# Optimization experiments

Measured on AMD Instinct MI355X. Metric: run time of the kernel, lower is better.

The kernel has to match this reference:

```python
import jax, jax.numpy as jnp
import numpy as np

RADIUS = 0.1
NSAMPLE = 32
EPS = 1e-5


def ball_query(radius, nsample, xyz):
    # xyz: [B, N, 3] -> idx [B, N, nsample] (query set == support set)
    B, N, _ = xyz.shape
    # pairwise squared distances [B, N, N]
    sq = jnp.sum((xyz[:, :, None, :] - xyz[:, None, :, :]) ** 2, axis=-1)
    grp = jnp.broadcast_to(jnp.arange(N, dtype=jnp.int32), (B, N, N))
    grp = jnp.where(sq > radius * radius, N, grp)
    grp = jnp.sort(grp, axis=-1)[:, :, :nsample]
    first = grp[:, :, 0:1]
    return jnp.where(grp == N, first, grp)  # self is always in-ball -> first valid


def index_points(points, idx):
    # points [B, N, C], idx [B, N, S] -> [B, N, S, C]
    B, N, S = idx.shape
    C = points.shape[-1]
    flat = jnp.take_along_axis(points, idx.reshape(B, N * S, 1), axis=1)
    return flat.reshape(B, N, S, C)


def bn(x, gamma, beta, mean, var, axis):
    # eval-mode batchnorm over channel axis
    shape = [1] * x.ndim
    shape[axis] = -1
    g = gamma.reshape(shape); b = beta.reshape(shape)
    m = mean.reshape(shape); v = var.reshape(shape)
    return (x - m) * (g * jax.lax.rsqrt(v + EPS)) + b


def setup_inputs() -> dict:
    key = jax.random.key(0)
    ks = jax.random.split(key, 8)
    B, N, C, E = 4, 4096, 128, 4
    H = C * E
    xyz = jax.random.uniform(ks[0], (B, N, 3), dtype=jnp.float32)
    feats = jax.random.normal(ks[1], (B, N, C), dtype=jnp.float32)
    s = 0.05
    Wn = jax.random.normal(ks[2], (C, C + 3), dtype=jnp.float32) * s
    W1 = jax.random.normal(ks[3], (H, C), dtype=jnp.float32) * s
    W2 = jax.random.normal(ks[4], (C, H), dtype=jnp.float32) * s
    def bnp(k, n):
        k1, k2 = jax.random.split(k)
        return (jnp.ones((n,), jnp.float32) + 0.01 * jax.random.normal(k1, (n,)),
                0.01 * jax.random.normal(k2, (n,)),
                jnp.zeros((n,), jnp.float32),
                jnp.ones((n,), jnp.float32))
    gn, bn_, mn, vn = bnp(ks[5], C)
    g1, b1, m1, v1 = bnp(ks[6], H)
    g2, b2, m2, v2 = bnp(ks[7], C)
    return dict(xyz=xyz, feats=feats, Wn=Wn, gn=gn, bn_=bn_, mn=mn, vn=vn,
                W1=W1, g1=g1, b1=b1, m1=m1, v1=v1,
                W2=W2, g2=g2, b2=b2, m2=m2, v2=v2)


def reference(xyz, feats, Wn, gn, bn_, mn, vn, W1, g1, b1, m1, v1, W2, g2, b2, m2, v2):
    B, N, C = feats.shape
    identity = feats  # [B, N, C]
    idx = ball_query(RADIUS, NSAMPLE, xyz)  # [B, N, S]
    grouped_xyz = index_points(xyz, idx) - xyz[:, :, None, :]  # [B, N, S, 3]
    grouped_xyz = grouped_xyz / RADIUS  # normalize_dp
    grouped_feats = index_points(feats, idx)  # [B, N, S, C]
    grouped = jnp.concatenate([grouped_xyz, grouped_feats], axis=-1)  # [B, N, S, C+3]
    # torch layout [B, C+3, S, N]; keep [B, N, S, C+3] and contract channels
    x = jnp.einsum('oc,bnsc->bnso', Wn, grouped)  # neighbor 1x1 conv
    x = jax.nn.relu(bn(x, gn, bn_, mn, vn, axis=3))
    x = jnp.max(x, axis=2)  # max over neighbors -> [B, N, C]
    # inverted bottleneck pointwise MLP
    h = jnp.einsum('hc,bnc->bnh', W1, x)
    h = jax.nn.relu(bn(h, g1, b1, m1, v1, axis=2))
    y = jnp.einsum('ch,bnh->bnc', W2, h)
    y = bn(y, g2, b2, m2, v2, axis=2)
    out = jax.nn.relu(y + identity)  # [B, N, C]
    return out
```

## Files before the change

### kernel.cpp

```cpp
#include <hip/hip_runtime.h>
#include <hip/hip_bf16.h>
#include <math.h>

static constexpr int BB = 4;
static constexpr int NN = 4096;
static constexpr int CC = 128;
static constexpr int HH = 512;
static constexpr int SS = 32;
static constexpr float EPSF = 1e-5f;
static constexpr int NCELL = 1000;

typedef __bf16 bf16_t;
typedef bf16_t bf16x8 __attribute__((ext_vector_type(8)));
typedef float f32x4 __attribute__((ext_vector_type(4)));
typedef float f32x2 __attribute__((ext_vector_type(2)));

__device__ inline unsigned short f2bf(float f) {
    unsigned int u = __builtin_bit_cast(unsigned int, f);
    u += 0x7FFFu + ((u >> 16) & 1u);
    return (unsigned short)(u >> 16);
}
__device__ inline float u2f(unsigned int u) {
    return __builtin_bit_cast(float, u);
}
__device__ inline int cell_of(float v) {
    int c = (int)(v * 10.0f);
    return c > 9 ? 9 : (c < 0 ? 0 : c);
}
__device__ inline f32x2 pk_fma_b(f32x2 a, float g, f32x2 c) {
    const f32x2 gg = {g, g};
    return a * gg + c;
}

__device__ inline void gload_lds16(const void* g, void* l) {
    __builtin_amdgcn_global_load_lds(
        (const __attribute__((address_space(1))) unsigned int*)g,
        (__attribute__((address_space(3))) unsigned int*)l, 16, 0, 0);
}

__global__ __launch_bounds__(1024)
void prep_bin_kernel(const float* __restrict__ Wn, const float* __restrict__ W1,
                     const float* __restrict__ W2,
                     const float* __restrict__ gn, const float* __restrict__ bnv,
                     const float* __restrict__ mn, const float* __restrict__ vn,
                     const float* __restrict__ xyz,
                     unsigned short* __restrict__ WnF, unsigned short* __restrict__ W1b,
                     unsigned short* __restrict__ W2b, float4* __restrict__ wfold,
                     int* __restrict__ starts, float4* __restrict__ spts)
{
    const int blk = blockIdx.x;
    const int t   = threadIdx.x;

    __shared__ int cur[1024];
    __shared__ int ls[1024];

    if (blk < 144) {
        const int i = blk * 1024 + t;
        if (i < 16384) {
            const int o = i >> 7, c = i & 127;
            WnF[i] = f2bf(Wn[o * 131 + 3 + c]);
        } else if (i < 81920) {
            W1b[i - 16384] = f2bf(W1[i - 16384]);
        } else {
            W2b[i - 81920] = f2bf(W2[i - 81920]);
        }
        return;
    }
    if (blk == 144) {
        if (t < CC) {
            const float sc = gn[t] / sqrtf(vn[t] + EPSF);
            wfold[t] = make_float4(sc * Wn[t * 131 + 0], sc * Wn[t * 131 + 1],
                                   sc * Wn[t * 131 + 2], bnv[t] - mn[t] * sc);
        }
        return;
    }

    const int b = blk - 145;
    cur[t] = 0;
    __syncthreads();

    int    cid[4];
    float4 pt[4];
    #pragma unroll
    for (int k = 0; k < 4; ++k) {
        const int n = k * 1024 + t;
        const float x = xyz[((size_t)b * NN + n) * 3 + 0];
        const float y = xyz[((size_t)b * NN + n) * 3 + 1];
        const float z = xyz[((size_t)b * NN + n) * 3 + 2];
        cid[k] = cell_of(z) * 100 + cell_of(y) * 10 + cell_of(x);
        pt[k]  = make_float4(x, y, z, __int_as_float(n));
        atomicAdd(&cur[cid[k]], 1);
    }
    __syncthreads();

    const int v = cur[t];
    ls[t] = v;
    __syncthreads();
    #pragma unroll
    for (int off = 1; off < 1024; off <<= 1) {
        const int add = (t >= off) ? ls[t - off] : 0;
        __syncthreads();
        ls[t] += add;
        __syncthreads();
    }
    const int ex = ls[t] - v;
    if (t < NCELL) starts[b * NCELL + t] = b * NN + ex;
    if (b == 0 && t == 0) starts[BB * NCELL] = BB * NN;
    __syncthreads();
    cur[t] = ex;
    __syncthreads();

    #pragma unroll
    for (int k = 0; k < 4; ++k) {
        const int pos = atomicAdd(&cur[cid[k]], 1);
        spts[(size_t)b * NN + pos] = pt[k];
    }
}

__global__ __launch_bounds__(256, 2)
void tgemm_bq_kernel(const float* __restrict__ feats, const unsigned short* __restrict__ WnF,
                     const float* __restrict__ gn, const float* __restrict__ vn,
                     unsigned short* __restrict__ Tb,
                     const float* __restrict__ xyz, const int* __restrict__ starts,
                     const float4* __restrict__ spts, int* __restrict__ idx)
{
    __shared__ char smem[(64 + 128) * 128];

    if (blockIdx.x < 256) {
        char* sA = smem;
        char* sB = smem + 64 * 128;
        const int t    = threadIdx.x;
        const int lane = t & 63;
        const int w    = t >> 6;
        const int wm   = w >> 1;
        const int wn   = w & 1;
        const int m0   = blockIdx.x * 64;

        f32x4 acc[2][4];
        #pragma unroll
        for (int i = 0; i < 2; ++i)
            #pragma unroll
            for (int j = 0; j < 4; ++j) acc[i][j] = f32x4{0.f, 0.f, 0.f, 0.f};

        const char* Wb = (const char*)WnF;

        for (int kc = 0; kc < CC; kc += 64) {
            #pragma unroll
            for (int l = 0; l < 2; ++l) {
                const int q     = w * 2 + l;
                const int Lb    = q * 1024 + lane * 16;
                const int row   = Lb >> 7;
                const int inrow = Lb & 127;
                const int sw    = inrow ^ ((row & 7) << 4);
                const float* src = feats + (size_t)(m0 + row) * CC + kc + (sw >> 1);
                const float4 a0 = *(const float4*)(src);
                const float4 a1 = *(const float4*)(src + 4);
                uint4 pk;
                pk.x = (unsigned)f2bf(a0.x) | ((unsigned)f2bf(a0.y) << 16);
                pk.y = (unsigned)f2bf(a0.z) | ((unsigned)f2bf(a0.w) << 16);
                pk.z = (unsigned)f2bf(a1.x) | ((unsigned)f2bf(a1.y) << 16);
                pk.w = (unsigned)f2bf(a1.z) | ((unsigned)f2bf(a1.w) << 16);
                *(uint4*)(sA + Lb) = pk;
            }
            #pragma unroll
            for (int l = 0; l < 4; ++l) {
                const int q     = w * 4 + l;
                const int Lb    = q * 1024 + lane * 16;
                const int row   = Lb >> 7;
                const int inrow = Lb & 127;
                const char* src = Wb + (size_t)row * 256 + kc * 2 + (inrow ^ ((row & 7) << 4));
                gload_lds16(src, sB + q * 1024);
            }
            __syncthreads();

            #pragma unroll
            for (int ks = 0; ks < 2; ++ks) {
                const int kbyte = ks * 64 + (lane >> 4) * 16;
                bf16x8 af[2], bf[4];
                #pragma unroll
                for (int i = 0; i < 2; ++i) {
                    const int r = wm * 32 + i * 16 + (lane & 15);
                    af[i] = *(const bf16x8*)(sA + r * 128 + (kbyte ^ ((r & 7) << 4)));
                }
                #pragma unroll
                for (int j = 0; j < 4; ++j) {
                    const int r = wn * 64 + j * 16 + (lane & 15);
                    bf[j] = *(const bf16x8*)(sB + r * 128 + (kbyte ^ ((r & 7) << 4)));
                }
                #pragma unroll
                for (int i = 0; i < 2; ++i)
                    #pragma unroll
                    for (int j = 0; j < 4; ++j)
                        acc[i][j] = __builtin_amdgcn_mfma_f32_16x16x32_bf16(af[i], bf[j], acc[i][j], 0, 0, 0);
            }
            __syncthreads();
        }

        #pragma unroll
        for (int j = 0; j < 4; ++j) {
            const int col = wn * 64 + j * 16 + (lane & 15);
            const float scg = gn[col] / sqrtf(vn[col] + EPSF);
            #pragma unroll
            for (int i = 0; i < 2; ++i) {
                const int rowb = m0 + wm * 32 + i * 16 + (lane >> 4) * 4;
                #pragma unroll
                for (int r = 0; r < 4; ++r)
                    Tb[(size_t)(rowb + r) * CC + col] = f2bf(acc[i][j][r] * scg);
            }
        }
    } else {
        const int t    = threadIdx.x;
        const int wv   = t >> 6;
        const int lane = t & 63;
        const int p    = (blockIdx.x - 256) * 4 + wv;
        const int b    = p >> 12;

        int* lbase = (int*)smem + wv * 160;
        int* list  = lbase;
        int* res   = lbase + 128;

        const float qx = xyz[p * 3 + 0];
        const float qy = xyz[p * 3 + 1];
        const float qz = xyz[p * 3 + 2];
        const int cx = cell_of(qx), cy = cell_of(qy), cz = cell_of(qz);
        const int xlo = cx > 0 ? cx - 1 : 0;
        const int xhi = cx < 9 ? cx + 1 : 9;

        int cnt = 0;
        for (int dz = -1; dz <= 1; ++dz) {
            const int z2 = cz + dz;
            if (z2 < 0 || z2 > 9) continue;
            for (int dy = -1; dy <= 1; ++dy) {
                const int y2 = cy + dy;
                if (y2 < 0 || y2 > 9) continue;
                const int base = b * NCELL + z2 * 100 + y2 * 10;
                const int lo = starts[base + xlo];
                const int hi = starts[base + xhi + 1];
                for (int j0 = lo; j0 < hi; j0 += 64) {
                    const int j = j0 + lane;
                    bool in = false;
                    int pi = 0;
                    if (j < hi) {
                        const float4 s = spts[j];
                        float sq;
                        {
                            #pragma clang fp contract(off)
                            const float dx  = qx - s.x;
                            const float dyv = qy - s.y;
                            const float dzv = qz - s.z;
                            sq = dx * dx + dyv * dyv + dzv * dzv;
                        }
                        in = (sq <= 0.01f);
                        pi = __float_as_int(s.w);
                    }
                    const unsigned long long mask = __ballot(in);
                    if (in) {
                        const int pos = cnt + __popcll(mask & ((1ull << lane) - 1ull));
                        if (pos < 128) list[pos] = pi;
                    }
                    cnt += (int)__popcll(mask);
                }
            }
        }
        __syncthreads();

        const int c = cnt < 128 ? cnt : 128;
        #pragma unroll
        for (int l0 = 0; l0 < 2; ++l0) {
            const int l = lane + l0 * 64;
            if (l < c) {
                const int v = list[l];
                int r = 0;
                for (int k = 0; k < c; ++k) r += (list[k] < v);
                if (r < SS) res[r] = v;
            }
        }
        __syncthreads();

        if (lane < SS) {
            const int m = c < SS ? c : SS;
            idx[(size_t)p * SS + lane] = (lane < m) ? res[lane] : res[0];
        }
    }
}

__global__ __launch_bounds__(256)
void group_max_kernel(const float* __restrict__ xyz,
                      const unsigned short* __restrict__ T,
                      const float4* __restrict__ wfold,
                      const int* __restrict__ idx, unsigned short* __restrict__ xout)
{
    const int t   = threadIdx.x;
    const int ptl = t >> 5;
    const int l   = t & 31;
    const int p   = blockIdx.x * 8 + ptl;
    const int b   = p >> 12;

    __shared__ float4 sg[8][32];

    {
        const int j = idx[(size_t)p * SS + l];
        const float* q  = xyz + (size_t)p * 3;
        const float* pj = xyz + ((size_t)b * NN + j) * 3;
        sg[ptl][l] = make_float4((pj[0] - q[0]) / 0.1f,
                                 (pj[1] - q[1]) / 0.1f,
                                 (pj[2] - q[2]) / 0.1f, __int_as_float(j));
    }
    __syncthreads();

    const int c0 = l * 4;
    const float4 wa = wfold[c0 + 0], wb = wfold[c0 + 1];
    const float4 wc = wfold[c0 + 2], wd = wfold[c0 + 3];
    const f32x2 w0p0 = {wa.x, wb.x}, w1p0 = {wa.y, wb.y}, w2p0 = {wa.z, wb.z};
    const f32x2 w0p1 = {wc.x, wd.x}, w1p1 = {wc.y, wd.y}, w2p1 = {wc.z, wd.z};

    const unsigned short* Tbp = T + (size_t)b * NN * CC;
    f32x2 mx0 = {-1e30f, -1e30f}, mx1 = {-1e30f, -1e30f};

    #pragma unroll 8
    for (int s = 0; s < SS; ++s) {
        const float4 g = sg[ptl][s];
        const int j = __float_as_int(g.w);
        const uint2 tv = *(const uint2*)(Tbp + (size_t)j * CC + c0);
        f32x2 v0, v1;
        v0.x = u2f(tv.x << 16); v0.y = u2f(tv.x & 0xFFFF0000u);
        v1.x = u2f(tv.y << 16); v1.y = u2f(tv.y & 0xFFFF0000u);
        v0 = pk_fma_b(w0p0, g.x, v0); v0 = pk_fma_b(w1p0, g.y, v0); v0 = pk_fma_b(w2p0, g.z, v0);
        v1 = pk_fma_b(w0p1, g.x, v1); v1 = pk_fma_b(w1p1, g.y, v1); v1 = pk_fma_b(w2p1, g.z, v1);
        mx0.x = fmaxf(mx0.x, v0.x); mx0.y = fmaxf(mx0.y, v0.y);
        mx1.x = fmaxf(mx1.x, v1.x); mx1.y = fmaxf(mx1.y, v1.y);
    }

    const float r0 = fmaxf(mx0.x + wa.w, 0.f);
    const float r1 = fmaxf(mx0.y + wb.w, 0.f);
    const float r2 = fmaxf(mx1.x + wc.w, 0.f);
    const float r3 = fmaxf(mx1.y + wd.w, 0.f);
    uint2 o;
    o.x = (unsigned)f2bf(r0) | ((unsigned)f2bf(r1) << 16);
    o.y = (unsigned)f2bf(r2) | ((unsigned)f2bf(r3) << 16);
    *(uint2*)(xout + (size_t)p * CC + c0) = o;
}

template<int MODE, int BNt>
__global__ __launch_bounds__(256, 2)
void mfma_gemm_kernel(const unsigned short* __restrict__ A, const unsigned short* __restrict__ W,
                      const float* __restrict__ g, const float* __restrict__ bb,
                      const float* __restrict__ mu, const float* __restrict__ var,
                      const float* __restrict__ res, void* __restrict__ outv,
                      int M, int Nout, int K)
{
    constexpr int BM = 64, BK = 64;
    constexpr int NF = BNt / 32;
    __shared__ char smem[(BM + BNt) * BK * 2];
    char* sA = smem;
    char* sB = smem + BM * BK * 2;

    const int t    = threadIdx.x;
    const int lane = t & 63;
    const int w    = t >> 6;
    const int wm   = w >> 1;
    const int wn   = w & 1;
    const int m0   = blockIdx.x * BM;
    const int o0   = blockIdx.y * BNt;
    const int Kb   = K * 2;

    f32x4 acc[2][NF];
    #pragma unroll
    for (int i = 0; i < 2; ++i)
        #pragma unroll
        for (int j = 0; j < NF; ++j) acc[i][j] = f32x4{0.f, 0.f, 0.f, 0.f};

    const char* Ab = (const char*)A;
    const char* Wb = (const char*)W;

    for (int kc = 0; kc < K; kc += BK) {
        const int kcb = kc * 2;
        #pragma unroll
        for (int l = 0; l < 2; ++l) {
            const int q     = w * 2 + l;
            const int Lb    = q * 1024 + lane * 16;
            const int row   = Lb >> 7;
            const int inrow = Lb & 127;
            const char* src = Ab + (size_t)(m0 + row) * Kb + kcb + (inrow ^ ((row & 7) << 4));
            gload_lds16(src, sA + q * 1024);
        }
        #pragma unroll
        for (int l = 0; l < NF; ++l) {
            const int q     = w * NF + l;
            const int Lb    = q * 1024 + lane * 16;
            const int row   = Lb >> 7;
            const int inrow = Lb & 127;
            const char* src = Wb + (size_t)(o0 + row) * Kb + kcb + (inrow ^ ((row & 7) << 4));
            gload_lds16(src, sB + q * 1024);
        }
        __syncthreads();

        #pragma unroll
        for (int ks = 0; ks < 2; ++ks) {
            const int kbyte = ks * 64 + (lane >> 4) * 16;
            bf16x8 af[2], bf[NF];
            #pragma unroll
            for (int i = 0; i < 2; ++i) {
                const int r = wm * 32 + i * 16 + (lane & 15);
                af[i] = *(const bf16x8*)(sA + r * 128 + (kbyte ^ ((r & 7) << 4)));
            }
            #pragma unroll
            for (int j = 0; j < NF; ++j) {
                const int r = wn * (BNt / 2) + j * 16 + (lane & 15);
                bf[j] = *(const bf16x8*)(sB + r * 128 + (kbyte ^ ((r & 7) << 4)));
            }
            #pragma unroll
            for (int i = 0; i < 2; ++i)
                #pragma unroll
                for (int j = 0; j < NF; ++j)
                    acc[i][j] = __builtin_amdgcn_mfma_f32_16x16x32_bf16(af[i], bf[j], acc[i][j], 0, 0, 0);
        }
        __syncthreads();
    }

    #pragma unroll
    for (int j = 0; j < NF; ++j) {
        const int col = o0 + wn * (BNt / 2) + j * 16 + (lane & 15);
        const float scg = g[col] / sqrtf(var[col] + EPSF);
        const float mm  = mu[col];
        const float sh  = bb[col];
        #pragma unroll
        for (int i = 0; i < 2; ++i) {
            const int rowb = m0 + wm * 32 + i * 16 + (lane >> 4) * 4;
            #pragma unroll
            for (int r = 0; r < 4; ++r) {
                float z = acc[i][j][r];
                z = (z - mm) * scg + sh;
                if constexpr (MODE == 2) z += res[(size_t)(rowb + r) * Nout + col];
                z = fmaxf(z, 0.f);
                if constexpr (MODE == 2)
                    ((float*)outv)[(size_t)(rowb + r) * Nout + col] = z;
                else
                    ((unsigned short*)outv)[(size_t)(rowb + r) * Nout + col] = f2bf(z);
            }
        }
    }
}

extern "C" void kernel_launch(void* const* d_in, const int* in_sizes, int n_in,
                              void* d_out, int out_size, void* d_ws, size_t ws_size,
                              hipStream_t stream)
{
    const float* xyz   = (const float*)d_in[0];
    const float* feats = (const float*)d_in[1];
    const float* Wn    = (const float*)d_in[2];
    const float* gn    = (const float*)d_in[3];
    const float* bn_   = (const float*)d_in[4];
    const float* mn    = (const float*)d_in[5];
    const float* vn    = (const float*)d_in[6];
    const float* W1    = (const float*)d_in[7];
    const float* g1    = (const float*)d_in[8];
    const float* b1    = (const float*)d_in[9];
    const float* m1    = (const float*)d_in[10];
    const float* v1    = (const float*)d_in[11];
    const float* W2    = (const float*)d_in[12];
    const float* g2    = (const float*)d_in[13];
    const float* b2    = (const float*)d_in[14];
    const float* m2    = (const float*)d_in[15];
    const float* v2    = (const float*)d_in[16];
    float* out = (float*)d_out;

    char* ws = (char*)d_ws;
    int*            idx    = (int*)(ws);
    int*            starts = (int*)(ws + 2097152);
    float4*         spts   = (float4*)(ws + 2113536);
    unsigned short* WnF    = (unsigned short*)(ws + 2375680);
    unsigned short* W1b    = (unsigned short*)(ws + 2408448);
    unsigned short* W2b    = (unsigned short*)(ws + 2539520);
    unsigned short* Tb     = (unsigned short*)(ws + 2670592);
    unsigned short* xb     = (unsigned short*)(ws + 6864896);
    unsigned short* hb     = (unsigned short*)(ws + 11059200);
    float4*         wfold  = (float4*)(ws + 27836416);

    const int M = BB * NN;

    prep_bin_kernel<<<149, 1024, 0, stream>>>(Wn, W1, W2, gn, bn_, mn, vn, xyz,
                                              WnF, W1b, W2b, wfold, starts, spts);

    tgemm_bq_kernel<<<256 + M / 4, 256, 0, stream>>>(feats, WnF, gn, vn, Tb,
                                                     xyz, starts, spts, idx);

    group_max_kernel<<<M / 8, 256, 0, stream>>>(xyz, Tb, wfold, idx, xb);

    mfma_gemm_kernel<1, 128><<<dim3(M / 64, HH / 128), 256, 0, stream>>>(
        xb, W1b, g1, b1, m1, v1, nullptr, hb, M, HH, CC);

    mfma_gemm_kernel<2, 64><<<dim3(M / 64, CC / 64), 256, 0, stream>>>(
        hb, W2b, g2, b2, m2, v2, feats, out, M, CC, HH);
}
```

Baseline: 151.0 us.

## Fuse group-max, expansion GEMM and projection GEMM into one kernel

Replaces the group-max kernel and both MLP GEMM kernels with a single kernel. Each block handles 64 points, computes the neighbor max into LDS, runs the 128->512 GEMM into an LDS-resident hidden tile, then runs the 512->128 GEMM with the residual epilogue. This removes the global round trips for the x and h intermediates and two launches. In exchange it uses 112KB of LDS with one block per CU, only 256 blocks, and no overlap between weight loads and MFMA, so latency hiding may suffer.

```diff
diff --git a/kernel.cpp b/kernel.cpp
--- a/kernel.cpp
+++ b/kernel.cpp
@@ -284,159 +284,201 @@
     }
 }
 
-__global__ __launch_bounds__(256)
-void group_max_kernel(const float* __restrict__ xyz,
+__global__ __launch_bounds__(256, 1)
+void fused_mlp_kernel(const float* __restrict__ xyz,
                       const unsigned short* __restrict__ T,
                       const float4* __restrict__ wfold,
-                      const int* __restrict__ idx, unsigned short* __restrict__ xout)
+                      const int* __restrict__ idx,
+                      const unsigned short* __restrict__ W1b,
+                      const float* __restrict__ g1, const float* __restrict__ b1,
+                      const float* __restrict__ m1, const float* __restrict__ v1,
+                      const unsigned short* __restrict__ W2b,
+                      const float* __restrict__ g2, const float* __restrict__ b2,
+                      const float* __restrict__ m2, const float* __restrict__ v2,
+                      const float* __restrict__ feats, float* __restrict__ out)
 {
-    const int t   = threadIdx.x;
-    const int ptl = t >> 5;
-    const int l   = t & 31;
-    const int p   = blockIdx.x * 8 + ptl;
-    const int b   = p >> 12;
-
-    __shared__ float4 sg[8][32];
-
-    {
-        const int j = idx[(size_t)p * SS + l];
-        const float* q  = xyz + (size_t)p * 3;
-        const float* pj = xyz + ((size_t)b * NN + j) * 3;
-        sg[ptl][l] = make_float4((pj[0] - q[0]) / 0.1f,
-                                 (pj[1] - q[1]) / 0.1f,
-                                 (pj[2] - q[2]) / 0.1f, __int_as_float(j));
-    }
-    __syncthreads();
-
-    const int c0 = l * 4;
-    const float4 wa = wfold[c0 + 0], wb = wfold[c0 + 1];
-    const float4 wc = wfold[c0 + 2], wd = wfold[c0 + 3];
-    const f32x2 w0p0 = {wa.x, wb.x}, w1p0 = {wa.y, wb.y}, w2p0 = {wa.z, wb.z};
-    const f32x2 w0p1 = {wc.x, wd.x}, w1p1 = {wc.y, wd.y}, w2p1 = {wc.z, wd.z};
-
-    const unsigned short* Tbp = T + (size_t)b * NN * CC;
-    f32x2 mx0 = {-1e30f, -1e30f}, mx1 = {-1e30f, -1e30f};
-
-    #pragma unroll 8
-    for (int s = 0; s < SS; ++s) {
-        const float4 g = sg[ptl][s];
-        const int j = __float_as_int(g.w);
-        const uint2 tv = *(const uint2*)(Tbp + (size_t)j * CC + c0);
-        f32x2 v0, v1;
-        v0.x = u2f(tv.x << 16); v0.y = u2f(tv.x & 0xFFFF0000u);
-        v1.x = u2f(tv.y << 16); v1.y = u2f(tv.y & 0xFFFF0000u);
-        v0 = pk_fma_b(w0p0, g.x, v0); v0 = pk_fma_b(w1p0, g.y, v0); v0 = pk_fma_b(w2p0, g.z, v0);
-        v1 = pk_fma_b(w0p1, g.x, v1); v1 = pk_fma_b(w1p1, g.y, v1); v1 = pk_fma_b(w2p1, g.z, v1);
-        mx0.x = fmaxf(mx0.x, v0.x); mx0.y = fmaxf(mx0.y, v0.y);
-        mx1.x = fmaxf(mx1.x, v1.x); mx1.y = fmaxf(mx1.y, v1.y);
-    }
-
-    const float r0 = fmaxf(mx0.x + wa.w, 0.f);
-    const float r1 = fmaxf(mx0.y + wb.w, 0.f);
-    const float r2 = fmaxf(mx1.x + wc.w, 0.f);
-    const float r3 = fmaxf(mx1.y + wd.w, 0.f);
-    uint2 o;
-    o.x = (unsigned)f2bf(r0) | ((unsigned)f2bf(r1) << 16);
-    o.y = (unsigned)f2bf(r2) | ((unsigned)f2bf(r3) << 16);
-    *(uint2*)(xout + (size_t)p * CC + c0) = o;
-}
-
-template<int MODE, int BNt>
-__global__ __launch_bounds__(256, 2)
-void mfma_gemm_kernel(const unsigned short* __restrict__ A, const unsigned short* __restrict__ W,
-                      const float* __restrict__ g, const float* __restrict__ bb,
-                      const float* __restrict__ mu, const float* __restrict__ var,
-                      const float* __restrict__ res, void* __restrict__ outv,
-                      int M, int Nout, int K)
-{
-    constexpr int BM = 64, BK = 64;
-    constexpr int NF = BNt / 32;
-    __shared__ char smem[(BM + BNt) * BK * 2];
-    char* sA = smem;
-    char* sB = smem + BM * BK * 2;
+    __shared__ char smem[114688];
+    char* hs  = smem;
+    char* ws2 = smem + 65536;
+    char* xs  = smem + 98304;
 
     const int t    = threadIdx.x;
+    const int m0   = blockIdx.x * 64;
+    const int b    = m0 >> 12;
     const int lane = t & 63;
     const int w    = t >> 6;
     const int wm   = w >> 1;
     const int wn   = w & 1;
-    const int m0   = blockIdx.x * BM;
-    const int o0   = blockIdx.y * BNt;
-    const int Kb   = K * 2;
-
-    f32x4 acc[2][NF];
+
+    {
+        float4* sg = (float4*)ws2;
+        const int ptl = t >> 5;
+        const int l   = t & 31;
+
+        #pragma unroll
+        for (int kp = 0; kp < 8; ++kp) {
+            const int pl = kp * 8 + ptl;
+            const int p  = m0 + pl;
+            const int j  = idx[(size_t)p * SS + l];
+            const float* q  = xyz + (size_t)p * 3;
+            const float* pj = xyz + ((size_t)b * NN + j) * 3;
+            sg[pl * 32 + l] = make_float4((pj[0] - q[0]) / 0.1f,
+                                          (pj[1] - q[1]) / 0.1f,
+                                          (pj[2] - q[2]) / 0.1f, __int_as_float(j));
+        }
+        __syncthreads();
+
+        const int c0 = l * 4;
+        const float4 wa = wfold[c0 + 0], wb = wfold[c0 + 1];
+        const float4 wc = wfold[c0 + 2], wd = wfold[c0 + 3];
+        const f32x2 w0p0 = {wa.x, wb.x}, w1p0 = {wa.y, wb.y}, w2p0 = {wa.z, wb.z};
+        const f32x2 w0p1 = {wc.x, wd.x}, w1p1 = {wc.y, wd.y}, w2p1 = {wc.z, wd.z};
+        const unsigned short* Tbp = T + (size_t)b * NN * CC;
+
+        for (int kp = 0; kp < 8; ++kp) {
+            const int pl = kp * 8 + ptl;
+            f32x2 mx0 = {-1e30f, -1e30f}, mx1 = {-1e30f, -1e30f};
+            #pragma unroll 8
+            for (int s = 0; s < SS; ++s) {
+                const float4 g = sg[pl * 32 + s];
+                const int j = __float_as_int(g.w);
+                const uint2 tv = *(const uint2*)(Tbp + (size_t)j * CC + c0);
+                f32x2 v0, v1;
+                v0.x = u2f(tv.x << 16); v0.y = u2f(tv.x & 0xFFFF0000u);
+                v1.x = u2f(tv.y << 16); v1.y = u2f(tv.y & 0xFFFF0000u);
+                v0 = pk_fma_b(w0p0, g.x, v0); v0 = pk_fma_b(w1p0, g.y, v0); v0 = pk_fma_b(w2p0, g.z, v0);
+                v1 = pk_fma_b(w0p1, g.x, v1); v1 = pk_fma_b(w1p1, g.y, v1); v1 = pk_fma_b(w2p1, g.z, v1);
+                mx0.x = fmaxf(mx0.x, v0.x); mx0.y = fmaxf(mx0.y, v0.y);
+                mx1.x = fmaxf(mx1.x, v1.x); mx1.y = fmaxf(mx1.y, v1.y);
+            }
+            const float r0 = fmaxf(mx0.x + wa.w, 0.f);
+            const float r1 = fmaxf(mx0.y + wb.w, 0.f);
+            const float r2 = fmaxf(mx1.x + wc.w, 0.f);
+            const float r3 = fmaxf(mx1.y + wd.w, 0.f);
+            uint2 o;
+            o.x = (unsigned)f2bf(r0) | ((unsigned)f2bf(r1) << 16);
+            o.y = (unsigned)f2bf(r2) | ((unsigned)f2bf(r3) << 16);
+            *(uint2*)(xs + pl * 256 + ((c0 * 2) ^ ((pl & 7) << 4))) = o;
+        }
+    }
+    __syncthreads();
+
+    for (int nc = 0; nc < 4; ++nc) {
+        #pragma unroll
+        for (int lq = 0; lq < 8; ++lq) {
+            const int Lb    = (lq * 256 + t) * 16;
+            const int row   = Lb >> 8;
+            const int inrow = Lb & 255;
+            const int sw    = inrow ^ ((row & 7) << 4);
+            gload_lds16((const char*)W1b + (size_t)(nc * 128 + row) * 256 + sw, ws2 + Lb);
+        }
+        __syncthreads();
+
+        f32x4 acc[2][4];
+        #pragma unroll
+        for (int i = 0; i < 2; ++i)
+            #pragma unroll
+            for (int j = 0; j < 4; ++j) acc[i][j] = f32x4{0.f, 0.f, 0.f, 0.f};
+
+        #pragma unroll
+        for (int kc = 0; kc < 2; ++kc) {
+            #pragma unroll
+            for (int ks = 0; ks < 2; ++ks) {
+                const int kbyte = kc * 128 + ks * 64 + (lane >> 4) * 16;
+                bf16x8 af[2], bf[4];
+                #pragma unroll
+                for (int i = 0; i < 2; ++i) {
+                    const int r = wm * 32 + i * 16 + (lane & 15);
+                    af[i] = *(const bf16x8*)(xs + r * 256 + (kbyte ^ ((r & 7) << 4)));
+                }
+                #pragma unroll
+                for (int j = 0; j < 4; ++j) {
+                    const int r = wn * 64 + j * 16 + (lane & 15);
+                    bf[j] = *(const bf16x8*)(ws2 + r * 256 + (kbyte ^ ((r & 7) << 4)));
+                }
+                #pragma unroll
+                for (int i = 0; i < 2; ++i)
+                    #pragma unroll
+                    for (int j = 0; j < 4; ++j)
+                        acc[i][j] = __builtin_amdgcn_mfma_f32_16x16x32_bf16(af[i], bf[j], acc[i][j], 0, 0, 0);
+            }
+        }
+
+        #pragma unroll
+        for (int j = 0; j < 4; ++j) {
+            const int col = nc * 128 + wn * 64 + j * 16 + (lane & 15);
+            const float scg = g1[col] / sqrtf(v1[col] + EPSF);
+            const float mm  = m1[col];
+            const float sh  = b1[col];
+            #pragma unroll
+            for (int i = 0; i < 2; ++i) {
+                const int rowb = wm * 32 + i * 16 + (lane >> 4) * 4;
+                #pragma unroll
+                for (int r = 0; r < 4; ++r) {
+                    const float z = fmaxf((acc[i][j][r] - mm) * scg + sh, 0.f);
+                    const int row = rowb + r;
+                    *(unsigned short*)(hs + row * 1024 + ((col * 2) ^ ((row & 7) << 4))) = f2bf(z);
+                }
+            }
+        }
+        __syncthreads();
+    }
+
+    f32x4 acc2[2][4];
     #pragma unroll
     for (int i = 0; i < 2; ++i)
         #pragma unroll
-        for (int j = 0; j < NF; ++j) acc[i][j] = f32x4{0.f, 0.f, 0.f, 0.f};
-
-    const char* Ab = (const char*)A;
-    const char* Wb = (const char*)W;
-
-    for (int kc = 0; kc < K; kc += BK) {
-        const int kcb = kc * 2;
-        #pragma unroll
-        for (int l = 0; l < 2; ++l) {
-            const int q     = w * 2 + l;
-            const int Lb    = q * 1024 + lane * 16;
+        for (int j = 0; j < 4; ++j) acc2[i][j] = f32x4{0.f, 0.f, 0.f, 0.f};
+
+    for (int kc = 0; kc < 8; ++kc) {
+        #pragma unroll
+        for (int lq = 0; lq < 4; ++lq) {
+            const int Lb    = (lq * 256 + t) * 16;
             const int row   = Lb >> 7;
             const int inrow = Lb & 127;
-            const char* src = Ab + (size_t)(m0 + row) * Kb + kcb + (inrow ^ ((row & 7) << 4));
-            gload_lds16(src, sA + q * 1024);
-        }
-        #pragma unroll
-        for (int l = 0; l < NF; ++l) {
-            const int q     = w * NF + l;
-            const int Lb    = q * 1024 + lane * 16;
-            const int row   = Lb >> 7;
-            const int inrow = Lb & 127;
-            const char* src = Wb + (size_t)(o0 + row) * Kb + kcb + (inrow ^ ((row & 7) << 4));
-            gload_lds16(src, sB + q * 1024);
+            const int sw    = inrow ^ ((row & 7) << 4);
+            gload_lds16((const char*)W2b + (size_t)row * 1024 + kc * 128 + sw, ws2 + Lb);
         }
         __syncthreads();
 
         #pragma unroll
         for (int ks = 0; ks < 2; ++ks) {
-            const int kbyte = ks * 64 + (lane >> 4) * 16;
-            bf16x8 af[2], bf[NF];
+            const int kb_hs = kc * 128 + ks * 64 + (lane >> 4) * 16;
+            const int kb_w  = ks * 64 + (lane >> 4) * 16;
+            bf16x8 af[2], bf[4];
             #pragma unroll
             for (int i = 0; i < 2; ++i) {
                 const int r = wm * 32 + i * 16 + (lane & 15);
-                af[i] = *(const bf16x8*)(sA + r * 128 + (kbyte ^ ((r & 7) << 4)));
-            }
-            #pragma unroll
-            for (int j = 0; j < NF; ++j) {
-                const int r = wn * (BNt / 2) + j * 16 + (lane & 15);
-                bf[j] = *(const bf16x8*)(sB + r * 128 + (kbyte ^ ((r & 7) << 4)));
+                af[i] = *(const bf16x8*)(hs + r * 1024 + (kb_hs ^ ((r & 7) << 4)));
+            }
+            #pragma unroll
+            for (int j = 0; j < 4; ++j) {
+                const int r = wn * 64 + j * 16 + (lane & 15);
+                bf[j] = *(const bf16x8*)(ws2 + r * 128 + (kb_w ^ ((r & 7) << 4)));
             }
             #pragma unroll
             for (int i = 0; i < 2; ++i)
                 #pragma unroll
-                for (int j = 0; j < NF; ++j)
-                    acc[i][j] = __builtin_amdgcn_mfma_f32_16x16x32_bf16(af[i], bf[j], acc[i][j], 0, 0, 0);
+                for (int j = 0; j < 4; ++j)
+                    acc2[i][j] = __builtin_amdgcn_mfma_f32_16x16x32_bf16(af[i], bf[j], acc2[i][j], 0, 0, 0);
         }
         __syncthreads();
     }
 
     #pragma unroll
-    for (int j = 0; j < NF; ++j) {
-        const int col = o0 + wn * (BNt / 2) + j * 16 + (lane & 15);
-        const float scg = g[col] / sqrtf(var[col] + EPSF);
-        const float mm  = mu[col];
-        const float sh  = bb[col];
+    for (int j = 0; j < 4; ++j) {
+        const int col = wn * 64 + j * 16 + (lane & 15);
+        const float scg = g2[col] / sqrtf(v2[col] + EPSF);
+        const float mm  = m2[col];
+        const float sh  = b2[col];
         #pragma unroll
         for (int i = 0; i < 2; ++i) {
             const int rowb = m0 + wm * 32 + i * 16 + (lane >> 4) * 4;
             #pragma unroll
             for (int r = 0; r < 4; ++r) {
-                float z = acc[i][j][r];
-                z = (z - mm) * scg + sh;
-                if constexpr (MODE == 2) z += res[(size_t)(rowb + r) * Nout + col];
-                z = fmaxf(z, 0.f);
-                if constexpr (MODE == 2)
-                    ((float*)outv)[(size_t)(rowb + r) * Nout + col] = z;
-                else
-                    ((unsigned short*)outv)[(size_t)(rowb + r) * Nout + col] = f2bf(z);
+                float z = (acc2[i][j][r] - mm) * scg + sh;
+                z += feats[(size_t)(rowb + r) * CC + col];
+                out[(size_t)(rowb + r) * CC + col] = fmaxf(z, 0.f);
             }
         }
     }
@@ -473,9 +515,7 @@
     unsigned short* W1b    = (unsigned short*)(ws + 2408448);
     unsigned short* W2b    = (unsigned short*)(ws + 2539520);
     unsigned short* Tb     = (unsigned short*)(ws + 2670592);
-    unsigned short* xb     = (unsigned short*)(ws + 6864896);
-    unsigned short* hb     = (unsigned short*)(ws + 11059200);
-    float4*         wfold  = (float4*)(ws + 27836416);
+    float4*         wfold  = (float4*)(ws + 6864896);
 
     const int M = BB * NN;
 
@@ -485,11 +525,8 @@
     tgemm_bq_kernel<<<256 + M / 4, 256, 0, stream>>>(feats, WnF, gn, vn, Tb,
                                                      xyz, starts, spts, idx);
 
-    group_max_kernel<<<M / 8, 256, 0, stream>>>(xyz, Tb, wfold, idx, xb);
-
-    mfma_gemm_kernel<1, 128><<<dim3(M / 64, HH / 128), 256, 0, stream>>>(
-        xb, W1b, g1, b1, m1, v1, nullptr, hb, M, HH, CC);
-
-    mfma_gemm_kernel<2, 64><<<dim3(M / 64, CC / 64), 256, 0, stream>>>(
-        hb, W2b, g2, b2, m2, v2, feats, out, M, CC, HH);
-}
+    fused_mlp_kernel<<<M / 64, 256, 0, stream>>>(xyz, Tb, wfold, idx,
+                                                 W1b, g1, b1, m1, v1,
+                                                 W2b, g2, b2, m2, v2,
+                                                 feats, out);
+}
```

Measured after the change: 155.8 us. 3.1% more time.
